# Optimization experiments

Measured on AMD Instinct MI355X. Metric: run time of the kernel, lower is better.

## Reference

```python
import jax, jax.numpy as jnp
import numpy as np

D_MODEL = 512
N_HEAD = 8
D_K = 64
D_V = 64
NUM_FEATURES = 266  # round(d_k * ln(d_k)) for d_k=64
KERNEL_EPS = 1e-4
NORM_STAB = 1e-6
LN_EPS = 1e-6


def _orthogonal_random_features():
    # blocks of transposed Q factors of Gaussian matrices, scaled by sqrt(d_k)
    rng = np.random.default_rng(0)
    blocks, rows = [], NUM_FEATURES
    while rows > 0:
        g = rng.standard_normal((D_K, D_K)).astype(np.float32)
        qm, _ = np.linalg.qr(g)
        blocks.append(qm.T[: min(rows, D_K)])
        rows -= D_K
    rf = np.concatenate(blocks, axis=0) * np.sqrt(D_K)
    return jnp.asarray(rf, dtype=jnp.float32)  # [m, d_k]


def _xavier(key, fan_in, fan_out):
    a = np.sqrt(6.0 / (fan_in + fan_out))
    return jax.random.uniform(key, (fan_in, fan_out), jnp.float32, -a, a)


def setup_inputs() -> dict:
    key = jax.random.key(0)
    ks = jax.random.split(key, 9)
    B, N = 1, 2048
    return {
        "q": jax.random.normal(ks[0], (B, N, D_MODEL), jnp.float32),
        "k": jax.random.normal(ks[1], (B, N, D_MODEL), jnp.float32),
        "v": jax.random.normal(ks[2], (B, N, D_MODEL), jnp.float32),
        "Wq": _xavier(ks[3], D_MODEL, N_HEAD * D_K),
        "Wk": _xavier(ks[4], D_MODEL, N_HEAD * D_K),
        "Wv": _xavier(ks[5], D_MODEL, N_HEAD * D_V),
        "W_fc": _xavier(ks[6], N_HEAD * D_V, D_MODEL),
        "b_fc": jnp.zeros((D_MODEL,), jnp.float32),
        "gamma": jnp.ones((D_MODEL,), jnp.float32),
        "beta": jnp.zeros((D_MODEL,), jnp.float32),
        "rf": _orthogonal_random_features(),
    }


def reference(q, k, v, Wq, Wk, Wv, W_fc, b_fc, gamma, beta, rf):
    B, N, _ = q.shape
    residual = q
    # pre-layernorm on queries only (normalize_before=True)
    mu = jnp.mean(q, axis=-1, keepdims=True)
    var = jnp.mean((q - mu) ** 2, axis=-1, keepdims=True)
    qn = (q - mu) * jax.lax.rsqrt(var + LN_EPS) * gamma + beta

    def heads(x, W, d):
        return (x @ W).reshape(B, N, N_HEAD, d).transpose(0, 2, 1, 3)

    qh = heads(qn, Wq, D_K)   # [b,h,n,dk]
    kh = heads(k, Wk, D_K)
    vh = heads(v, Wv, D_V)    # [b,h,n,dv]

    scale = D_MODEL ** (-0.25)
    qh = qh * scale
    kh = kh * scale

    proj_q = jnp.einsum('bhnd,md->bhnm', qh, rf)  # [b,h,n,m]
    proj_k = jnp.einsum('bhnd,md->bhnm', kh, rf)
    h_q = -0.5 * jnp.sum(qh ** 2, axis=-1, keepdims=True)  # [b,h,n,1]
    h_k = -0.5 * jnp.sum(kh ** 2, axis=-1, keepdims=True)

    # per-query stabilizer is h_q itself (last dim of h_q has size 1)
    q_kernel = jnp.exp(h_q + (proj_q - h_q))
    k_stab = jnp.max(h_k)  # global max stabilizer for keys
    k_kernel = jnp.exp(h_k + (proj_k - k_stab))

    c = NUM_FEATURES ** (-0.5)
    q_prime = c * (q_kernel + KERNEL_EPS)
    k_prime = c * (k_kernel + KERNEL_EPS)

    # causal linear attention via prefix sums
    D_inv = 1.0 / jnp.einsum('bhnm,bhnm->bhn', q_prime, jnp.cumsum(k_prime, axis=2))
    context = jnp.cumsum(jnp.einsum('bhnm,bhne->bhnme', k_prime, vh), axis=2)  # [b,h,n,m,dv]
    out = jnp.einsum('bhnme,bhnm,bhn->bhne', context, q_prime, D_inv)

    # output normalization with stabilizer
    d = jnp.einsum('bhnm,bhm->bhn', q_prime, jnp.sum(k_prime, axis=2))[..., None]
    d = d + 2.0 * NORM_STAB * (jnp.abs(d) <= NORM_STAB).astype(d.dtype)
    out = out / d

    out = out.transpose(0, 2, 1, 3).reshape(B, N, N_HEAD * D_V)
    return out @ W_fc + b_fc + residual
```

## Files before the change

### kernel.cpp

```cpp
#include <hip/hip_runtime.h>
#include <hip/hip_bf16.h>
#include <math.h>

#define DMODEL 512
#define NSEQ 2048
#define NHEAD 8
#define DK 64
#define DV 64
#define MFEAT 266
#define MPAD 288
#define NT 32
#define LN_EPS 1e-6f
#define KERNEL_EPS 1e-4f
#define NORM_STAB 1e-6f
#define SCALE 0.21022410381342863f

typedef __attribute__((ext_vector_type(8))) short short8;
typedef __attribute__((ext_vector_type(4))) short sv4;
typedef __attribute__((ext_vector_type(4))) float f32x4;

__device__ inline short f2bf(float f) {
    return (short)__bfloat16_as_ushort(__float2bfloat16(f));
}
__device__ inline float bf2f(short s) {
    unsigned u = ((unsigned)(unsigned short)s) << 16;
    return __builtin_bit_cast(float, u);
}

__global__ __launch_bounds__(256) void prep_kernel(const float* __restrict__ Wq,
                                                   const float* __restrict__ Wk,
                                                   const float* __restrict__ Wv,
                                                   const float* __restrict__ Wfc,
                                                   short* __restrict__ Wqt,
                                                   short* __restrict__ Wkt,
                                                   short* __restrict__ Wvt,
                                                   short* __restrict__ Wfct) {
    __shared__ short T[64][65];
    int k0 = blockIdx.x * 64, n0 = blockIdx.y * 64, wsel = blockIdx.z;
    const float* W = (wsel == 0) ? Wq : (wsel == 1) ? Wk : (wsel == 2) ? Wv : Wfc;
    short* Wt = (wsel == 0) ? Wqt : (wsel == 1) ? Wkt : (wsel == 2) ? Wvt : Wfct;
    float scale = (wsel <= 1) ? SCALE : 1.f;
    int tid = threadIdx.x;
    for (int lp = 0; lp < 4; ++lp) {
        int c = tid + lp * 256;
        int kk = c >> 4, q4 = (c & 15) * 4;
        f32x4 v = *(const f32x4*)&W[(size_t)(k0 + kk) * DMODEL + n0 + q4];
        for (int j = 0; j < 4; ++j) T[q4 + j][kk] = f2bf(v[j] * scale);
    }
    __syncthreads();
    for (int lp = 0; lp < 2; ++lp) {
        int c = tid + lp * 256;
        int nn = c >> 3, c8 = c & 7;
        short8 v = *(const short8*)&T[nn][c8 * 8];
        *(short8*)&Wt[(size_t)(n0 + nn) * DMODEL + k0 + c8 * 8] = v;
    }
}

__global__ __launch_bounds__(256) void qkvfeat_kernel(const float* __restrict__ qx,
                                                      const float* __restrict__ kx,
                                                      const float* __restrict__ vx,
                                                      const short* __restrict__ Wqt,
                                                      const short* __restrict__ Wkt,
                                                      const short* __restrict__ Wvt,
                                                      const float* __restrict__ gamma,
                                                      const float* __restrict__ beta,
                                                      const float* __restrict__ rf,
                                                      short* __restrict__ vh,
                                                      short* __restrict__ qp,
                                                      short* __restrict__ kp) {
    __shared__ __align__(16) char smem[38656];
    auto As = (short(*)[40])smem;
    auto Bs = (short(*)[40])(smem + 5120);
    auto Xs = (short(*)[72])smem;
    short* kpl = (short*)smem;
    float* hks = (float*)(smem + 38400);

    int z = blockIdx.z;
    const float* A = (z == 0) ? qx : (z == 1) ? kx : vx;
    const short* Bt = (z == 0) ? Wqt : (z == 1) ? Wkt : Wvt;
    int nt = blockIdx.x, h = blockIdx.y;
    int bm = nt * 64, bn = h * 64, n0 = nt * 64;
    int tid = threadIdx.x;
    int wid = tid >> 6, lane = tid & 63;
    f32x4 acc[4] = {f32x4{0,0,0,0}, f32x4{0,0,0,0}, f32x4{0,0,0,0}, f32x4{0,0,0,0}};
    int ar = tid >> 2, akq = tid & 3;
    float lnm = 0.f, lnr = 0.f;
    if (z == 0) {
        const float* xr = qx + (size_t)(bm + ar) * DMODEL + akq * 128;
        float s = 0.f, ss = 0.f;
#pragma unroll 4
        for (int i = 0; i < 128; i += 4) {
            f32x4 vv = *(const f32x4*)(xr + i);
            s += vv[0] + vv[1] + vv[2] + vv[3];
            ss += vv[0]*vv[0] + vv[1]*vv[1] + vv[2]*vv[2] + vv[3]*vv[3];
        }
        s += __shfl_xor(s, 1); s += __shfl_xor(s, 2);
        ss += __shfl_xor(ss, 1); ss += __shfl_xor(ss, 2);
        float m = s / (float)DMODEL;
        float var = ss / (float)DMODEL - m * m;
        lnm = m;
        lnr = rsqrtf(var + LN_EPS);
    }
    for (int k0 = 0; k0 < DMODEL; k0 += 32) {
        {
            const float* src = A + (size_t)(bm + ar) * DMODEL + k0 + akq * 8;
            f32x4 v0 = *(const f32x4*)src;
            f32x4 v1 = *(const f32x4*)(src + 4);
            short8 sv;
            if (z == 0) {
                f32x4 g0 = *(const f32x4*)&gamma[k0 + akq * 8];
                f32x4 g1 = *(const f32x4*)&gamma[k0 + akq * 8 + 4];
                f32x4 bb0 = *(const f32x4*)&beta[k0 + akq * 8];
                f32x4 bb1 = *(const f32x4*)&beta[k0 + akq * 8 + 4];
                for (int j = 0; j < 4; ++j) {
                    sv[j] = f2bf((v0[j] - lnm) * lnr * g0[j] + bb0[j]);
                    sv[4 + j] = f2bf((v1[j] - lnm) * lnr * g1[j] + bb1[j]);
                }
            } else {
                for (int j = 0; j < 4; ++j) { sv[j] = f2bf(v0[j]); sv[4 + j] = f2bf(v1[j]); }
            }
            *(short8*)&As[ar][akq * 8] = sv;
        }
        {
            *(short8*)&Bs[ar][akq * 8] =
                *(const short8*)&Bt[(size_t)(bn + ar) * DMODEL + k0 + akq * 8];
        }
        __syncthreads();
        int row = wid * 16 + (lane & 15);
        int koff = (lane >> 4) * 8;
        short8 a = *(const short8*)&As[row][koff];
        for (int nf = 0; nf < 4; ++nf) {
            int col = nf * 16 + (lane & 15);
            short8 b = *(const short8*)&Bs[col][koff];
            acc[nf] = __builtin_amdgcn_mfma_f32_16x16x32_bf16(a, b, acc[nf], 0, 0, 0);
        }
        __syncthreads();
    }
    if (z == 2) {
        for (int nf = 0; nf < 4; ++nf) {
            int col = bn + nf * 16 + (lane & 15);
            for (int j = 0; j < 4; ++j) {
                int row = bm + wid * 16 + (lane >> 4) * 4 + j;
                vh[(size_t)row * DMODEL + col] = f2bf(acc[nf][j]);
            }
        }
        return;
    }
    for (int nf = 0; nf < 4; ++nf) {
        int col = nf * 16 + (lane & 15);
        for (int j = 0; j < 4; ++j) {
            int row = wid * 16 + (lane >> 4) * 4 + j;
            Xs[row][col] = f2bf(acc[nf][j]);
        }
    }
    if (z == 1) {
        for (int j = 0; j < 4; ++j) {
            float ss = 0.f;
            for (int nf = 0; nf < 4; ++nf) ss += acc[nf][j] * acc[nf][j];
            for (int o = 1; o < 16; o <<= 1) ss += __shfl_xor(ss, o);
            if ((lane & 15) == 0) hks[wid * 16 + (lane >> 4) * 4 + j] = -0.5f * ss;
        }
    }
    __syncthreads();

    int w = wid, l = lane;
    int fr = l & 15, fq = (l >> 4) * 8;
    short8 xb0 = *(const short8*)&Xs[w * 16 + fr][fq];
    short8 xb1 = *(const short8*)&Xs[w * 16 + fr][32 + fq];
    int n_loc = w * 16 + fr;
    float hval = (z == 1) ? hks[n_loc] : 0.f;
    __syncthreads();

    short (*kpl2)[300] = (short(*)[300])kpl;
    const float cnorm = 0.06131393394849658f;
#pragma unroll
    for (int tr = 0; tr < 18; ++tr) {
        int row = tr * 16 + fr;
        short8 a0, a1;
        if (row < MFEAT) {
            const float* rp = rf + (size_t)row * DK;
            f32x4 v0 = *(const f32x4*)(rp + fq);
            f32x4 v1 = *(const f32x4*)(rp + fq + 4);
            f32x4 v2 = *(const f32x4*)(rp + 32 + fq);
            f32x4 v3 = *(const f32x4*)(rp + 32 + fq + 4);
            for (int j = 0; j < 4; ++j) {
                a0[j] = f2bf(v0[j]); a0[4 + j] = f2bf(v1[j]);
                a1[j] = f2bf(v2[j]); a1[4 + j] = f2bf(v3[j]);
            }
        } else {
            for (int j = 0; j < 8; ++j) { a0[j] = 0; a1[j] = 0; }
        }
        f32x4 facc = {0.f, 0.f, 0.f, 0.f};
        facc = __builtin_amdgcn_mfma_f32_16x16x32_bf16(a0, xb0, facc, 0, 0, 0);
        facc = __builtin_amdgcn_mfma_f32_16x16x32_bf16(a1, xb1, facc, 0, 0, 0);
        sv4 o;
        for (int j = 0; j < 4; ++j) {
            int m = tr * 16 + (l >> 4) * 4 + j;
            float val = (m < MFEAT) ? cnorm * (__expf(facc[j] + hval) + KERNEL_EPS) : 0.f;
            o[j] = f2bf(val);
        }
        *(sv4*)&kpl2[n_loc][tr * 16 + (l >> 4) * 4] = o;
    }
    __syncthreads();
    short* outp = (z == 0) ? qp : kp;
    for (int lp = 0; lp < 9; ++lp) {
        int c = tid + lp * 256;
        int nn = c / 36, c8 = c % 36;
        short8 v = *(const short8*)&kpl2[nn][c8 * 8];
        *(short8*)&outp[((size_t)h * NSEQ + n0 + nn) * MPAD + c8 * 8] = v;
    }
}

__global__ __launch_bounds__(256) void chunksum_kernel(const short* __restrict__ kp,
                                                       const short* __restrict__ vh,
                                                       short* __restrict__ KVc,
                                                       float* __restrict__ Ks) {
    int t = blockIdx.x, h = blockIdx.y;
    __shared__ short kpT[288 * 72];
    __shared__ short Vt[64][72];
    int tid = threadIdx.x;
    int w = tid >> 6, l = tid & 63;
    int fr = l & 15, fq8 = (l >> 4) * 8;
    const short* kpb = kp + ((size_t)h * NSEQ + (size_t)t * 64) * MPAD;

    for (int lp = 0; lp < 9; ++lp) {
        int c = tid + lp * 256;
        int i = c / 36, c8 = c % 36;
        short8 v = *(const short8*)&kpb[(size_t)i * MPAD + c8 * 8];
        int i8 = i >> 3, i7 = i & 7;
        for (int jj = 0; jj < 8; ++jj) {
            int m = c8 * 8 + jj;
            int ig = i8 ^ ((m >> 3) & 7);
            kpT[m * 72 + ig * 8 + i7] = v[jj];
        }
    }
    for (int lp = 0; lp < 2; ++lp) {
        int c = tid + lp * 256;
        int i = c & 63, d8 = (c >> 6) * 8;
        short8 v = *(const short8*)&vh[(size_t)(t * 64 + i) * DMODEL + h * DV + d8];
        for (int jj = 0; jj < 8; ++jj) Vt[d8 + jj][i] = v[jj];
    }
    __syncthreads();

    f32x4 acc[5][4];
#pragma unroll
    for (int tt = 0; tt < 5; ++tt)
        for (int nf = 0; nf < 4; ++nf) acc[tt][nf] = f32x4{0, 0, 0, 0};
#pragma unroll
    for (int tt = 0; tt < 5; ++tt) {
        int tr = w + tt * 4;
        if (tr < 18) {
            int row = tr * 16 + fr;
            int swz = (row >> 3) & 7;
            short8 a0 = *(const short8*)&kpT[row * 72 + (((fq8 >> 3)) ^ swz) * 8];
            short8 a1 = *(const short8*)&kpT[row * 72 + ((4 + (fq8 >> 3)) ^ swz) * 8];
            for (int nf = 0; nf < 4; ++nf) {
                short8 b0 = *(const short8*)&Vt[nf * 16 + fr][fq8];
                short8 b1 = *(const short8*)&Vt[nf * 16 + fr][32 + fq8];
                acc[tt][nf] = __builtin_amdgcn_mfma_f32_16x16x32_bf16(a0, b0, acc[tt][nf], 0, 0, 0);
                acc[tt][nf] = __builtin_amdgcn_mfma_f32_16x16x32_bf16(a1, b1, acc[tt][nf], 0, 0, 0);
            }
        }
    }
    for (int m = tid; m < MPAD; m += 256) {
        int swz = (m >> 3) & 7;
        float s = 0.f;
        for (int i8 = 0; i8 < 8; ++i8) {
            int ig = i8 ^ swz;
            for (int j = 0; j < 8; ++j) s += bf2f(kpT[m * 72 + ig * 8 + j]);
        }
        Ks[((size_t)h * NT + t) * MPAD + m] = s;
    }
    __syncthreads();
    short* kvT = kpT;
#pragma unroll
    for (int tt = 0; tt < 5; ++tt) {
        int tr = w + tt * 4;
        if (tr < 18) {
            for (int nf = 0; nf < 4; ++nf) {
                int dv = nf * 16 + fr;
                for (int j = 0; j < 4; ++j) {
                    int m = tr * 16 + (l >> 4) * 4 + j;
                    kvT[dv * 296 + m] = f2bf(acc[tt][nf][j]);
                }
            }
        }
    }
    __syncthreads();
    for (int lp = 0; lp < 9; ++lp) {
        int c = tid + lp * 256;
        int dv = c / 36, c8 = c % 36;
        short8 v = *(const short8*)&kvT[dv * 296 + c8 * 8];
        *(short8*)&KVc[(((size_t)h * NT + t) * DV + dv) * MPAD + c8 * 8] = v;
    }
}

__global__ __launch_bounds__(256) void scan_kernel(const short* __restrict__ KVc,
                                                   short* __restrict__ KVbT,
                                                   float* __restrict__ Ks,
                                                   float* __restrict__ Ktot) {
    int idx = blockIdx.x * 256 + threadIdx.x;
    const int NKV = NHEAD * DV * MPAD;
    if (idx < NKV) {
        int h = idx / (DV * MPAD);
        int rem = idx % (DV * MPAD);
        size_t base = (size_t)h * NT * DV * MPAD + rem;
        short vals[NT];
#pragma unroll
        for (int t = 0; t < NT; ++t) vals[t] = KVc[base + (size_t)t * DV * MPAD];
        float run = 0.f;
#pragma unroll
        for (int t = 0; t < NT; ++t) {
            KVbT[base + (size_t)t * DV * MPAD] = f2bf(run);
            run += bf2f(vals[t]);
        }
    } else {
        int j = idx - NKV;
        if (j < NHEAD * MPAD) {
            int h = j / MPAD, m = j % MPAD;
            size_t base = (size_t)h * NT * MPAD + m;
            float vals[NT];
#pragma unroll
            for (int t = 0; t < NT; ++t) vals[t] = Ks[base + (size_t)t * MPAD];
            float run = 0.f;
#pragma unroll
            for (int t = 0; t < NT; ++t) {
                Ks[base + (size_t)t * MPAD] = run;
                run += vals[t];
            }
            Ktot[(size_t)h * MPAD + m] = run;
        }
    }
}

__global__ __launch_bounds__(256) void phasec_kernel(const short* __restrict__ qp,
                                                     const short* __restrict__ kp,
                                                     const short* __restrict__ vh,
                                                     const short* __restrict__ KVbT,
                                                     const float* __restrict__ Ks,
                                                     const float* __restrict__ Ktot,
                                                     short* __restrict__ attn) {
    int t = blockIdx.x, h = blockIdx.y;
    __shared__ short Buf[64][296];
    __shared__ short Vt[64][72];
    __shared__ short Am[64][72];
    __shared__ float Ksp[MPAD], Ktp[MPAD];
    __shared__ float fscale_s[64];
    int tid = threadIdx.x;
    int w = tid >> 6, l = tid & 63;
    int fr = l & 15, fq = (l >> 4) * 8;
    const short* qpb = qp + ((size_t)h * NSEQ + (size_t)t * 64) * MPAD;
    const short* kpb = kp + ((size_t)h * NSEQ + (size_t)t * 64) * MPAD;
    const short* stb = KVbT + ((size_t)h * NT + t) * DV * MPAD;

    short8 qf[9];
#pragma unroll
    for (int ks = 0; ks < 9; ++ks)
        qf[ks] = *(const short8*)&qpb[(size_t)(w * 16 + fr) * MPAD + ks * 32 + fq];

    int srow = tid >> 2, sc4 = tid & 3;
#pragma unroll
    for (int lp = 0; lp < 9; ++lp) {
        int c = sc4 + lp * 4;
        *(short8*)&Buf[srow][c * 8] = *(const short8*)&kpb[(size_t)srow * MPAD + c * 8];
    }
    for (int lp = 0; lp < 2; ++lp) {
        int c = tid + lp * 256;
        int i = c & 63, d8 = (c >> 6) * 8;
        short8 v = *(const short8*)&vh[(size_t)(t * 64 + i) * DMODEL + h * DV + d8];
        for (int jj = 0; jj < 8; ++jj) Vt[d8 + jj][i] = v[jj];
    }
    for (int idx = tid; idx < MPAD; idx += 256) {
        Ksp[idx] = Ks[((size_t)h * NT + t) * MPAD + idx];
        Ktp[idx] = Ktot[(size_t)h * MPAD + idx];
    }
    short8 stg[9];
#pragma unroll
    for (int lp = 0; lp < 9; ++lp) {
        int c = sc4 + lp * 4;
        stg[lp] = *(const short8*)&stb[(size_t)srow * MPAD + c * 8];
    }
    __syncthreads();

    f32x4 accA[4] = {f32x4{0,0,0,0}, f32x4{0,0,0,0}, f32x4{0,0,0,0}, f32x4{0,0,0,0}};
    f32x4 accO[4] = {f32x4{0,0,0,0}, f32x4{0,0,0,0}, f32x4{0,0,0,0}, f32x4{0,0,0,0}};
#pragma unroll 3
    for (int ks = 0; ks < 9; ++ks) {
        int ko = ks * 32 + fq;
        for (int nf = 0; nf < 4; ++nf) {
            short8 bk = *(const short8*)&Buf[nf * 16 + fr][ko];
            accA[nf] = __builtin_amdgcn_mfma_f32_16x16x32_bf16(qf[ks], bk, accA[nf], 0, 0, 0);
        }
    }
    __syncthreads();
#pragma unroll
    for (int lp = 0; lp < 9; ++lp) {
        int c = sc4 + lp * 4;
        *(short8*)&Buf[srow][c * 8] = stg[lp];
    }
    for (int nf = 0; nf < 4; ++nf) {
        int col = nf * 16 + fr;
        for (int j = 0; j < 4; ++j) {
            int row = w * 16 + (l >> 4) * 4 + j;
            Am[row][col] = (col <= row) ? f2bf(accA[nf][j]) : (short)0;
        }
    }
    __syncthreads();
#pragma unroll 3
    for (int ks = 0; ks < 9; ++ks) {
        int ko = ks * 32 + fq;
        for (int nf = 0; nf < 4; ++nf) {
            short8 bs = *(const short8*)&Buf[nf * 16 + fr][ko];
            accO[nf] = __builtin_amdgcn_mfma_f32_16x16x32_bf16(qf[ks], bs, accO[nf], 0, 0, 0);
        }
    }
#pragma unroll
    for (int ks = 0; ks < 2; ++ks) {
        int ko = ks * 32 + fq;
        short8 a = *(const short8*)&Am[w * 16 + fr][ko];
        for (int nf = 0; nf < 4; ++nf) {
            short8 b = *(const short8*)&Vt[nf * 16 + fr][ko];
            accO[nf] = __builtin_amdgcn_mfma_f32_16x16x32_bf16(a, b, accO[nf], 0, 0, 0);
        }
    }
    int di = tid >> 2, dp = tid & 3;
    float dc = 0.f, df = 0.f;
    {
        const short* amrow = &Am[di][dp * 16];
        short8 s0 = *(const short8*)amrow;
        short8 s1 = *(const short8*)(amrow + 8);
        for (int j2 = 0; j2 < 8; ++j2) dc += bf2f(s0[j2]) + bf2f(s1[j2]);
    }
#pragma unroll
    for (int c8 = 0; c8 < 9; ++c8) {
        int m = dp * 72 + c8 * 8;
        short8 qv = *(const short8*)&qpb[(size_t)di * MPAD + m];
        for (int j2 = 0; j2 < 8; ++j2) {
            float qq = bf2f(qv[j2]);
            dc += qq * Ksp[m + j2];
            df += qq * Ktp[m + j2];
        }
    }
    dc += __shfl_xor(dc, 1); dc += __shfl_xor(dc, 2);
    df += __shfl_xor(df, 1); df += __shfl_xor(df, 2);
    if (dp == 0) {
        float dst = df;
        if (fabsf(dst) <= NORM_STAB) dst += 2.f * NORM_STAB;
        fscale_s[di] = (1.f / dc) / dst;
    }
    __syncthreads();
    for (int nf = 0; nf < 4; ++nf) {
        int col = nf * 16 + fr;
        for (int j = 0; j < 4; ++j) {
            int row = w * 16 + (l >> 4) * 4 + j;
            attn[((size_t)t * 64 + row) * DMODEL + h * DV + col] =
                f2bf(accO[nf][j] * fscale_s[row]);
        }
    }
}

__global__ __launch_bounds__(256) void fgemm_kernel(const short* __restrict__ A,
                                                    const short* __restrict__ Bt,
                                                    float* __restrict__ C,
                                                    const float* __restrict__ bias,
                                                    const float* __restrict__ residual) {
    __shared__ short As[64][40];
    __shared__ short Bs[64][40];
    int bm = blockIdx.y * 64, bn = blockIdx.x * 64;
    int tid = threadIdx.x;
    int wid = tid >> 6, lane = tid & 63;
    f32x4 acc[4] = {f32x4{0,0,0,0}, f32x4{0,0,0,0}, f32x4{0,0,0,0}, f32x4{0,0,0,0}};
    int ar = tid >> 2, akq = tid & 3;
    for (int k0 = 0; k0 < DMODEL; k0 += 32) {
        *(short8*)&As[ar][akq * 8] =
            *(const short8*)&A[(size_t)(bm + ar) * DMODEL + k0 + akq * 8];
        *(short8*)&Bs[ar][akq * 8] =
            *(const short8*)&Bt[(size_t)(bn + ar) * DMODEL + k0 + akq * 8];
        __syncthreads();
        int row = wid * 16 + (lane & 15);
        int koff = (lane >> 4) * 8;
        short8 a = *(const short8*)&As[row][koff];
        for (int nf = 0; nf < 4; ++nf) {
            int col = nf * 16 + (lane & 15);
            short8 b = *(const short8*)&Bs[col][koff];
            acc[nf] = __builtin_amdgcn_mfma_f32_16x16x32_bf16(a, b, acc[nf], 0, 0, 0);
        }
        __syncthreads();
    }
    for (int nf = 0; nf < 4; ++nf) {
        int col = bn + nf * 16 + (lane & 15);
        for (int j = 0; j < 4; ++j) {
            int row = bm + wid * 16 + (lane >> 4) * 4 + j;
            C[(size_t)row * DMODEL + col] =
                acc[nf][j] + bias[col] + residual[(size_t)row * DMODEL + col];
        }
    }
}

extern "C" void kernel_launch(void* const* d_in, const int* in_sizes, int n_in,
                              void* d_out, int out_size, void* d_ws, size_t ws_size,
                              hipStream_t stream) {
    const float* q = (const float*)d_in[0];
    const float* k = (const float*)d_in[1];
    const float* v = (const float*)d_in[2];
    const float* Wq = (const float*)d_in[3];
    const float* Wk = (const float*)d_in[4];
    const float* Wv = (const float*)d_in[5];
    const float* Wfc = (const float*)d_in[6];
    const float* bfc = (const float*)d_in[7];
    const float* gamma = (const float*)d_in[8];
    const float* beta = (const float*)d_in[9];
    const float* rf = (const float*)d_in[10];
    float* out = (float*)d_out;

    float* ws = (float*)d_ws;
    short* attn = (short*)ws;
    short* vhb = attn + (size_t)NSEQ * DMODEL;
    short* qp = vhb + (size_t)NSEQ * DMODEL;
    short* kp = qp + (size_t)NHEAD * NSEQ * MPAD;
    short* KVc = kp + (size_t)NHEAD * NSEQ * MPAD;
    short* KVbT = KVc + (size_t)NHEAD * NT * DV * MPAD;
    float* Ks = (float*)(KVbT + (size_t)NHEAD * NT * DV * MPAD);
    float* Ktot = Ks + (size_t)NHEAD * NT * MPAD;
    short* Wqt = (short*)(Ktot + (size_t)NHEAD * MPAD);
    short* Wkt = Wqt + (size_t)DMODEL * DMODEL;
    short* Wvt = Wkt + (size_t)DMODEL * DMODEL;
    short* Wfct = Wvt + (size_t)DMODEL * DMODEL;

    dim3 gp(8, 8, 4);
    prep_kernel<<<gp, 256, 0, stream>>>(Wq, Wk, Wv, Wfc, Wqt, Wkt, Wvt, Wfct);
    dim3 gq(NT, NHEAD, 3);
    qkvfeat_kernel<<<gq, 256, 0, stream>>>(q, k, v, Wqt, Wkt, Wvt, gamma, beta, rf,
                                           vhb, qp, kp);
    dim3 ga(NT, NHEAD);
    chunksum_kernel<<<ga, 256, 0, stream>>>(kp, vhb, KVc, Ks);
    int scan_threads = NHEAD * DV * MPAD + NHEAD * MPAD;
    scan_kernel<<<(scan_threads + 255) / 256, 256, 0, stream>>>(KVc, KVbT, Ks, Ktot);
    dim3 gc(NT, NHEAD);
    phasec_kernel<<<gc, 256, 0, stream>>>(qp, kp, vhb, KVbT, Ks, Ktot, attn);
    dim3 g(DMODEL / 64, NSEQ / 64);
    fgemm_kernel<<<g, 256, 0, stream>>>(attn, Wfct, out, bfc, q);
}
```

Baseline: 80.07 us.

## Double-buffer LDS tiles with register prefetch in projection and output GEMMs

Both the QKV/feature projection GEMM and the final output GEMM now keep two LDS tile buffers and prefetch the next K-slice from global memory into registers while the current slice is being multiplied. This drops one __syncthreads per iteration and lets global load latency overlap the MFMA work. In exchange it doubles the LDS tile footprint and raises register pressure from the prefetched values. The qkvfeat kernel's second buffer sits inside the existing shared allocation.

```diff
diff --git a/kernel.cpp b/kernel.cpp
--- a/kernel.cpp
+++ b/kernel.cpp
@@ -69,8 +69,8 @@
                                                       short* __restrict__ qp,
                                                       short* __restrict__ kp) {
     __shared__ __align__(16) char smem[38656];
-    auto As = (short(*)[40])smem;
-    auto Bs = (short(*)[40])(smem + 5120);
+    auto AsB = (short(*)[40])smem;
+    auto BsB = (short(*)[40])(smem + 10240);
     auto Xs = (short(*)[72])smem;
     short* kpl = (short*)smem;
     float* hks = (float*)(smem + 38400);
@@ -101,41 +101,47 @@
         lnm = m;
         lnr = rsqrtf(var + LN_EPS);
     }
+    auto loadA = [&](int k0) -> short8 {
+        const float* src = A + (size_t)(bm + ar) * DMODEL + k0 + akq * 8;
+        f32x4 v0 = *(const f32x4*)src;
+        f32x4 v1 = *(const f32x4*)(src + 4);
+        short8 sv;
+        if (z == 0) {
+            f32x4 g0 = *(const f32x4*)&gamma[k0 + akq * 8];
+            f32x4 g1 = *(const f32x4*)&gamma[k0 + akq * 8 + 4];
+            f32x4 bb0 = *(const f32x4*)&beta[k0 + akq * 8];
+            f32x4 bb1 = *(const f32x4*)&beta[k0 + akq * 8 + 4];
+            for (int j = 0; j < 4; ++j) {
+                sv[j] = f2bf((v0[j] - lnm) * lnr * g0[j] + bb0[j]);
+                sv[4 + j] = f2bf((v1[j] - lnm) * lnr * g1[j] + bb1[j]);
+            }
+        } else {
+            for (int j = 0; j < 4; ++j) { sv[j] = f2bf(v0[j]); sv[4 + j] = f2bf(v1[j]); }
+        }
+        return sv;
+    };
+    auto loadB = [&](int k0) -> short8 {
+        return *(const short8*)&Bt[(size_t)(bn + ar) * DMODEL + k0 + akq * 8];
+    };
+    short8 aReg = loadA(0), bReg = loadB(0);
+    int buf = 0;
+#pragma unroll 2
     for (int k0 = 0; k0 < DMODEL; k0 += 32) {
-        {
-            const float* src = A + (size_t)(bm + ar) * DMODEL + k0 + akq * 8;
-            f32x4 v0 = *(const f32x4*)src;
-            f32x4 v1 = *(const f32x4*)(src + 4);
-            short8 sv;
-            if (z == 0) {
-                f32x4 g0 = *(const f32x4*)&gamma[k0 + akq * 8];
-                f32x4 g1 = *(const f32x4*)&gamma[k0 + akq * 8 + 4];
-                f32x4 bb0 = *(const f32x4*)&beta[k0 + akq * 8];
-                f32x4 bb1 = *(const f32x4*)&beta[k0 + akq * 8 + 4];
-                for (int j = 0; j < 4; ++j) {
-                    sv[j] = f2bf((v0[j] - lnm) * lnr * g0[j] + bb0[j]);
-                    sv[4 + j] = f2bf((v1[j] - lnm) * lnr * g1[j] + bb1[j]);
-                }
-            } else {
-                for (int j = 0; j < 4; ++j) { sv[j] = f2bf(v0[j]); sv[4 + j] = f2bf(v1[j]); }
-            }
-            *(short8*)&As[ar][akq * 8] = sv;
-        }
-        {
-            *(short8*)&Bs[ar][akq * 8] =
-                *(const short8*)&Bt[(size_t)(bn + ar) * DMODEL + k0 + akq * 8];
-        }
+        *(short8*)&AsB[buf * 64 + ar][akq * 8] = aReg;
+        *(short8*)&BsB[buf * 64 + ar][akq * 8] = bReg;
         __syncthreads();
-        int row = wid * 16 + (lane & 15);
+        if (k0 + 32 < DMODEL) { aReg = loadA(k0 + 32); bReg = loadB(k0 + 32); }
+        int row = buf * 64 + wid * 16 + (lane & 15);
         int koff = (lane >> 4) * 8;
-        short8 a = *(const short8*)&As[row][koff];
+        short8 a = *(const short8*)&AsB[row][koff];
         for (int nf = 0; nf < 4; ++nf) {
-            int col = nf * 16 + (lane & 15);
-            short8 b = *(const short8*)&Bs[col][koff];
+            int col = buf * 64 + nf * 16 + (lane & 15);
+            short8 b = *(const short8*)&BsB[col][koff];
             acc[nf] = __builtin_amdgcn_mfma_f32_16x16x32_bf16(a, b, acc[nf], 0, 0, 0);
         }
-        __syncthreads();
-    }
+        buf ^= 1;
+    }
+    __syncthreads();
     if (z == 2) {
         for (int nf = 0; nf < 4; ++nf) {
             int col = bn + nf * 16 + (lane & 15);
@@ -464,28 +470,34 @@
                                                     float* __restrict__ C,
                                                     const float* __restrict__ bias,
                                                     const float* __restrict__ residual) {
-    __shared__ short As[64][40];
-    __shared__ short Bs[64][40];
+    __shared__ short AsB[128][40];
+    __shared__ short BsB[128][40];
     int bm = blockIdx.y * 64, bn = blockIdx.x * 64;
     int tid = threadIdx.x;
     int wid = tid >> 6, lane = tid & 63;
     f32x4 acc[4] = {f32x4{0,0,0,0}, f32x4{0,0,0,0}, f32x4{0,0,0,0}, f32x4{0,0,0,0}};
     int ar = tid >> 2, akq = tid & 3;
+    short8 aReg = *(const short8*)&A[(size_t)(bm + ar) * DMODEL + akq * 8];
+    short8 bReg = *(const short8*)&Bt[(size_t)(bn + ar) * DMODEL + akq * 8];
+    int buf = 0;
+#pragma unroll 2
     for (int k0 = 0; k0 < DMODEL; k0 += 32) {
-        *(short8*)&As[ar][akq * 8] =
-            *(const short8*)&A[(size_t)(bm + ar) * DMODEL + k0 + akq * 8];
-        *(short8*)&Bs[ar][akq * 8] =
-            *(const short8*)&Bt[(size_t)(bn + ar) * DMODEL + k0 + akq * 8];
+        *(short8*)&AsB[buf * 64 + ar][akq * 8] = aReg;
+        *(short8*)&BsB[buf * 64 + ar][akq * 8] = bReg;
         __syncthreads();
-        int row = wid * 16 + (lane & 15);
+        if (k0 + 32 < DMODEL) {
+            aReg = *(const short8*)&A[(size_t)(bm + ar) * DMODEL + k0 + 32 + akq * 8];
+            bReg = *(const short8*)&Bt[(size_t)(bn + ar) * DMODEL + k0 + 32 + akq * 8];
+        }
+        int row = buf * 64 + wid * 16 + (lane & 15);
         int koff = (lane >> 4) * 8;
-        short8 a = *(const short8*)&As[row][koff];
+        short8 a = *(const short8*)&AsB[row][koff];
         for (int nf = 0; nf < 4; ++nf) {
-            int col = nf * 16 + (lane & 15);
-            short8 b = *(const short8*)&Bs[col][koff];
+            int col = buf * 64 + nf * 16 + (lane & 15);
+            short8 b = *(const short8*)&BsB[col][koff];
             acc[nf] = __builtin_amdgcn_mfma_f32_16x16x32_bf16(a, b, acc[nf], 0, 0, 0);
         }
-        __syncthreads();
+        buf ^= 1;
     }
     for (int nf = 0; nf < 4; ++nf) {
         int col = bn + nf * 16 + (lane & 15);
```

Measured after the change: 76.74 us. -4.2%, faster.
